# Performance work log

Measured on AMD Instinct MI355X. Metric: run time of the kernel, lower is better.

Reference implementation:

```python
import jax, jax.numpy as jnp
import numpy as np

N_DRUG = 25000
N_DIS = 25000
N = N_DRUG + N_DIS
E = 800000
D_IN = 128
D_OUT = 128


def setup_inputs() -> dict:
    key = jax.random.key(0)
    k1, k2, k3, k4, k5, k6 = jax.random.split(key, 6)
    drug_f = jax.random.normal(k1, (N_DRUG, D_IN), dtype=jnp.float32)
    disease_f = jax.random.normal(k2, (N_DIS, D_IN), dtype=jnp.float32)
    rows = jax.random.randint(k3, (E,), 0, N, dtype=jnp.int64)
    cols = jax.random.randint(k4, (E,), 0, N, dtype=jnp.int64)
    # xavier_uniform_ equivalent for [D_IN, D_OUT]
    limit = float(np.sqrt(6.0 / (D_IN + D_OUT)))
    drug_w = jax.random.uniform(k5, (D_IN, D_OUT), minval=-limit, maxval=limit, dtype=jnp.float32)
    disease_w = jax.random.uniform(k6, (D_IN, D_OUT), minval=-limit, maxval=limit, dtype=jnp.float32)
    return {"drug_f": drug_f, "disease_f": disease_f, "drug_w": drug_w,
            "disease_w": disease_w, "rows": rows, "cols": cols}


def reference(drug_f, disease_f, drug_w, disease_w, rows, cols):
    # per-type linear projection
    drug_h = drug_f @ drug_w          # [n_drug, D_OUT]
    dis_h = disease_f @ disease_w     # [n_dis,  D_OUT]
    node_f = jnp.concatenate([drug_h, dis_h], axis=0)  # [N, D_OUT]
    # row-sum degrees of the (unit-valued) sparse adjacency, clamped at 1
    deg = jax.ops.segment_sum(jnp.ones((rows.shape[0],), node_f.dtype), rows,
                              num_segments=N)
    norm = jnp.clip(deg, 1.0, None) ** -0.5           # [N]
    # symmetric norm: norm * (A @ (norm * x)); SpMM as gather + segment_sum
    node_f = node_f * norm[:, None]
    msgs = node_f[cols]                               # [E, D_OUT]
    node_f = jax.ops.segment_sum(msgs, rows, num_segments=N)
    node_f = node_f * norm[:, None]
    return node_f
```

## Files before the change

kernel.cpp:

```cpp
#include <hip/hip_runtime.h>
#include <hip/hip_bf16.h>

#define D 128
#define CAP 64
#define BINSH 7
#define NSHARD 8
#define NCHUNK 384
#define PART_EDGES 4096

typedef short short8 __attribute__((ext_vector_type(8)));
typedef unsigned short ushort8 __attribute__((ext_vector_type(8)));
typedef float f32x4  __attribute__((ext_vector_type(4)));

__device__ __forceinline__ short f2bf(float x) {
    __hip_bfloat16 b = __float2bfloat16(x);
    return *reinterpret_cast<short*>(&b);
}
__device__ __forceinline__ float bf2f(unsigned short u) {
    return __uint_as_float((unsigned)u << 16);
}

__device__ __forceinline__ void wprep_block(int b16, int tid,
                                            const float* __restrict__ w0,
                                            const float* __restrict__ w1,
                                            __hip_bfloat16* __restrict__ wb) {
    int gid = b16 * 256 + tid;
    int type = gid >> 11;
    int tri  = gid & 2047;
    int lane = tri & 63;
    int ts   = tri >> 6;
    int s = ts & 3, t = ts >> 2;
    const float* W = type ? w1 : w0;
    int n = t * 16 + (lane & 15);
    int kbase = s * 32 + (lane >> 4) * 8;
    short8 v;
    #pragma unroll
    for (int j = 0; j < 8; ++j)
        v[j] = f2bf(W[(size_t)(kbase + j) * D + n]);
    *(short8*)&wb[(size_t)type * 16384 + (size_t)tri * 8] = v;
}

__global__ __launch_bounds__(256) void prep_sort_kernel(const float* __restrict__ w0,
                                                        const float* __restrict__ w1,
                                                        __hip_bfloat16* __restrict__ wb,
                                                        int* __restrict__ bincur, int nbin) {
    int b = blockIdx.x;
    if (b < 16) { wprep_block(b, threadIdx.x, w0, w1, wb); return; }
    for (int i = threadIdx.x; i < nbin; i += 256) bincur[i] = 0;
}

__global__ __launch_bounds__(256) void part_proj_kernel(
    const int* __restrict__ rows, const int* __restrict__ cols,
    int* __restrict__ bincur, unsigned int* __restrict__ payload,
    int E, int nbin, int capbin, int nparts,
    const float* __restrict__ f0, const float* __restrict__ f1,
    const __hip_bfloat16* __restrict__ wb,
    __hip_bfloat16* __restrict__ h,
    int n0, int n1, int nb0) {

    __shared__ short8 Wl[2048];
    int b = blockIdx.x;
    int t = threadIdx.x;

    if (b < nparts) {
        int* hist = (int*)&Wl[0];
        int* base = hist + 512;
        int* cur  = hist + 1024;
        int lo = b * PART_EDGES;
        int hi = lo + PART_EDGES; if (hi > E) hi = E;

        for (int i = t; i < nbin; i += 256) hist[i] = 0;
        __syncthreads();
        for (int i = lo + t; i < hi; i += 256)
            atomicAdd(&hist[rows[i] >> BINSH], 1);
        __syncthreads();
        for (int i = t; i < nbin; i += 256) {
            int c = hist[i];
            base[i] = (c > 0) ? atomicAdd(&bincur[i], c) : 0;
            cur[i] = 0;
        }
        __syncthreads();
        for (int i = lo + t; i < hi; i += 256) {
            int r = rows[i];
            int bn = r >> BINSH;
            int p = base[bn] + atomicAdd(&cur[bn], 1);
            if (p < capbin)
                payload[(size_t)bn * capbin + p] = ((unsigned)r << 16) | (unsigned)(cols[i] & 0xffff);
        }
        return;
    }

    int pb = b - nparts;
    int type = (pb >= nb0) ? 1 : 0;
    const float* f = type ? f1 : f0;
    int lbase = (type ? (pb - nb0) : pb) * 64;
    int nloc  = type ? n1 : n0;
    int goff  = type ? n0 : 0;

    const short8* src = (const short8*)wb + (size_t)type * 2048;
    for (int i = t; i < 2048; i += 256) Wl[i] = src[i];
    __syncthreads();

    int wave = t >> 6;
    int lane = t & 63;
    int m  = lane & 15;
    int kg = lane >> 4;
    int wrow = lbase + wave * 16;

    int arow = wrow + m;
    int arc = (arow < nloc) ? arow : (nloc - 1);
    const float* fr = f + (size_t)arc * D + kg * 8;
    short8 A[4];
    #pragma unroll
    for (int s = 0; s < 4; ++s) {
        float4 x = *(const float4*)(fr + s * 32);
        float4 y = *(const float4*)(fr + s * 32 + 4);
        short8 a;
        a[0] = f2bf(x.x); a[1] = f2bf(x.y); a[2] = f2bf(x.z); a[3] = f2bf(x.w);
        a[4] = f2bf(y.x); a[5] = f2bf(y.y); a[6] = f2bf(y.z); a[7] = f2bf(y.w);
        A[s] = a;
    }

    #pragma unroll
    for (int tt = 0; tt < 8; ++tt) {
        f32x4 acc = {0.f, 0.f, 0.f, 0.f};
        #pragma unroll
        for (int s = 0; s < 4; ++s)
            acc = __builtin_amdgcn_mfma_f32_16x16x32_bf16(A[s], Wl[(tt * 4 + s) * 64 + lane], acc, 0, 0, 0);
        #pragma unroll
        for (int r = 0; r < 4; ++r) {
            int grow = wrow + kg * 4 + r;
            if (grow < nloc)
                h[(size_t)(goff + grow) * D + tt * 16 + m] = __float2bfloat16(acc[r]);
        }
    }
}

__global__ __launch_bounds__(256) void binfill_kernel(const unsigned int* __restrict__ payload,
                                                      const int* __restrict__ bincur,
                                                      unsigned short* __restrict__ bucket,
                                                      int* __restrict__ cnt,
                                                      float* __restrict__ normf,
                                                      int capbin, int N) {
    __shared__ int rc[128];
    int b = blockIdx.x;
    int t = threadIdx.x;
    if (t < 128) rc[t] = 0;
    __syncthreads();
    int cntb = bincur[b]; if (cntb > capbin) cntb = capbin;
    const unsigned int* pp = payload + (size_t)b * capbin;
    for (int i = t; i < cntb; i += 256) {
        unsigned pay = pp[i];
        int rl = (pay >> 16) & 127;
        int p = atomicAdd(&rc[rl], 1);
        if (p < CAP)
            bucket[(size_t)((b << BINSH) | rl) * CAP + p] = (unsigned short)(pay & 0xffff);
    }
    __syncthreads();
    if (t < 128) {
        int r = (b << BINSH) | t;
        if (r < N) {
            int c = rc[t];
            cnt[r] = c;
            normf[r] = rsqrtf((float)(c < 1 ? 1 : c));
        }
    }
}

__global__ __launch_bounds__(256) void agg_kernel(const int* __restrict__ cnt,
                                                  const float* __restrict__ normf,
                                                  const unsigned short* __restrict__ bucket,
                                                  const __hip_bfloat16* __restrict__ h,
                                                  float* __restrict__ out, int n) {
    int wave = threadIdx.x >> 6;
    int lane = threadIdx.x & 63;
    int r = blockIdx.x * 4 + wave;
    if (r >= n) return;
    int d = cnt[r]; if (d > CAP) d = CAP;
    int s = r * CAP;

    int col = (int)bucket[s + lane];
    int cs  = (lane < d) ? col : 0;
    float wl = (lane < d) ? normf[cs] : 0.f;

    int g  = lane >> 4;
    int sl = lane & 15;

    float acc[8] = {0.f,0.f,0.f,0.f,0.f,0.f,0.f,0.f};
    for (int j = 0; j < d; j += 4) {
        int e = j + g;
        float we = __shfl(wl, e & 63); if (e >= d) we = 0.f;
        int   ce = __shfl(cs, e & 63);
        ushort8 v = *(const ushort8*)&h[(size_t)ce * D + sl * 8];
        #pragma unroll
        for (int k = 0; k < 8; ++k)
            acc[k] += we * bf2f(v[k]);
    }
    #pragma unroll
    for (int k = 0; k < 8; ++k) {
        acc[k] += __shfl_xor(acc[k], 16);
        acc[k] += __shfl_xor(acc[k], 32);
    }
    if (g == 0) {
        float nr = normf[r];
        float* po = &out[(size_t)r * D + sl * 8];
        *(float4*)po       = make_float4(acc[0]*nr, acc[1]*nr, acc[2]*nr, acc[3]*nr);
        *(float4*)(po + 4) = make_float4(acc[4]*nr, acc[5]*nr, acc[6]*nr, acc[7]*nr);
    }
}

__global__ __launch_bounds__(256) void prep_kernel(const float* __restrict__ w0,
                                                   const float* __restrict__ w1,
                                                   __hip_bfloat16* __restrict__ wb,
                                                   int* __restrict__ cnt, int N) {
    int b = blockIdx.x;
    if (b < 16) { wprep_block(b, threadIdx.x, w0, w1, wb); }
    else {
        int i = (b - 16) * 256 + threadIdx.x;
        if (i < N) cnt[i] = 0;
    }
}

__global__ __launch_bounds__(256) void fill_shard_kernel(const int* __restrict__ rows,
                                                         const int* __restrict__ cols,
                                                         int* __restrict__ cnt,
                                                         unsigned short* __restrict__ bucket,
                                                         int E, int shsz, int ch) {
    int s     = blockIdx.x & (NSHARD - 1);
    int chunk = blockIdx.x >> 3;
    int lo = chunk * ch;
    int hi = lo + ch; if (hi > E) hi = E;
    int rlo = s * shsz;
    for (int i = lo + (int)threadIdx.x; i < hi; i += 256) {
        int r = rows[i];
        if ((unsigned)(r - rlo) < (unsigned)shsz) {
            int p = atomicAdd(&cnt[r], 1);
            if (p < CAP) bucket[(size_t)r * CAP + p] = (unsigned short)cols[i];
        }
    }
}

__global__ void norm_from_cnt_kernel(const int* __restrict__ cnt, float* __restrict__ normf, int N) {
    int i = blockIdx.x * 256 + threadIdx.x;
    if (i < N) { int c = cnt[i]; normf[i] = rsqrtf((float)(c < 1 ? 1 : c)); }
}

extern "C" void kernel_launch(void* const* d_in, const int* in_sizes, int n_in,
                              void* d_out, int out_size, void* d_ws, size_t ws_size,
                              hipStream_t stream) {
    const float* drug_f    = (const float*)d_in[0];
    const float* disease_f = (const float*)d_in[1];
    const float* drug_w    = (const float*)d_in[2];
    const float* disease_w = (const float*)d_in[3];
    const int*   rows      = (const int*)d_in[4];
    const int*   cols      = (const int*)d_in[5];
    float* out = (float*)d_out;

    int n_drug = in_sizes[0] / D;
    int n_dis  = in_sizes[1] / D;
    int N = n_drug + n_dis;
    int E = in_sizes[4];
    (void)out_size; (void)n_in;

    char* ws = (char*)d_ws;
    size_t off = 0;
    auto alloc = [&](size_t bytes) { void* p = ws + off; off = (off + bytes + 255) & ~(size_t)255; return p; };

    int*            cnt      = (int*)alloc(sizeof(int) * N);
    float*          normf    = (float*)alloc(sizeof(float) * N);
    __hip_bfloat16* h_raw    = (__hip_bfloat16*)alloc(sizeof(__hip_bfloat16) * (size_t)N * D);
    __hip_bfloat16* wb       = (__hip_bfloat16*)alloc(sizeof(__hip_bfloat16) * 2 * 16384);
    unsigned short* bucket   = (unsigned short*)alloc((size_t)N * CAP * sizeof(unsigned short));

    int nb0 = (n_drug + 63) / 64;
    int nb1 = (n_dis + 63) / 64;

    int nbin   = (N + (1 << BINSH) - 1) >> BINSH;
    int capbin = (((E / nbin) * 3 / 2) + 63) & ~63;
    size_t sort_need = off
        + ((sizeof(int) * nbin + 255) & ~(size_t)255)
        + ((sizeof(unsigned int) * (size_t)nbin * capbin + 255) & ~(size_t)255);

    if (ws_size >= sort_need && nbin <= 512) {
        int*          bincur  = (int*)alloc(sizeof(int) * nbin);
        unsigned int* payload = (unsigned int*)alloc(sizeof(unsigned int) * (size_t)nbin * capbin);

        int nparts = (E + PART_EDGES - 1) / PART_EDGES;
        prep_sort_kernel<<<17, 256, 0, stream>>>(drug_w, disease_w, wb, bincur, nbin);
        part_proj_kernel<<<nparts + nb0 + nb1, 256, 0, stream>>>(
            rows, cols, bincur, payload, E, nbin, capbin, nparts,
            drug_f, disease_f, wb, h_raw, n_drug, n_dis, nb0);
        binfill_kernel<<<nbin, 256, 0, stream>>>(payload, bincur, bucket, cnt, normf, capbin, N);
        agg_kernel<<<(N + 3) / 4, 256, 0, stream>>>(cnt, normf, bucket, h_raw, out, N);
    } else {
        int shsz = (N + NSHARD - 1) / NSHARD;
        int ch   = (E + NCHUNK - 1) / NCHUNK;
        int prep_blocks = 16 + (N + 255) / 256;

        prep_kernel<<<prep_blocks, 256, 0, stream>>>(drug_w, disease_w, wb, cnt, N);
        fill_shard_kernel<<<NCHUNK * NSHARD, 256, 0, stream>>>(rows, cols, cnt, bucket, E, shsz, ch);
        norm_from_cnt_kernel<<<(N + 255) / 256, 256, 0, stream>>>(cnt, normf, N);
        part_proj_kernel<<<nb0 + nb1, 256, 0, stream>>>(
            rows, cols, (int*)nullptr, (unsigned int*)nullptr, E, nbin, capbin, 0,
            drug_f, disease_f, wb, h_raw, n_drug, n_dis, nb0);
        agg_kernel<<<(N + 3) / 4, 256, 0, stream>>>(cnt, normf, bucket, h_raw, out, N);
    }
}
```

Before: 71.17 us.

## Use nontemporal loads/stores for streamed data and stage bucket fill in LDS

Streamed single-use data (rows, cols, features, payload, bucket, output) now goes through nontemporal load and store builtins, so it is less likely to evict the reused projected features h from cache. binfill now scatters each bin's columns into a zeroed shared-memory tile and writes the whole 128x64 bucket block out with coalesced vector stores, instead of scattered 2-byte global writes. This adds 16KB of LDS per block, which may lower occupancy, and writes the full tile including unused slots.

```diff
diff --git a/kernel.cpp b/kernel.cpp
--- a/kernel.cpp
+++ b/kernel.cpp
@@ -72,7 +72,7 @@
         for (int i = t; i < nbin; i += 256) hist[i] = 0;
         __syncthreads();
         for (int i = lo + t; i < hi; i += 256)
-            atomicAdd(&hist[rows[i] >> BINSH], 1);
+            atomicAdd(&hist[__builtin_nontemporal_load(&rows[i]) >> BINSH], 1);
         __syncthreads();
         for (int i = t; i < nbin; i += 256) {
             int c = hist[i];
@@ -81,11 +81,12 @@
         }
         __syncthreads();
         for (int i = lo + t; i < hi; i += 256) {
-            int r = rows[i];
+            int r = __builtin_nontemporal_load(&rows[i]);
+            int c = __builtin_nontemporal_load(&cols[i]);
             int bn = r >> BINSH;
             int p = base[bn] + atomicAdd(&cur[bn], 1);
             if (p < capbin)
-                payload[(size_t)bn * capbin + p] = ((unsigned)r << 16) | (unsigned)(cols[i] & 0xffff);
+                payload[(size_t)bn * capbin + p] = ((unsigned)r << 16) | (unsigned)(c & 0xffff);
         }
         return;
     }
@@ -113,11 +114,11 @@
     short8 A[4];
     #pragma unroll
     for (int s = 0; s < 4; ++s) {
-        float4 x = *(const float4*)(fr + s * 32);
-        float4 y = *(const float4*)(fr + s * 32 + 4);
+        f32x4 x = __builtin_nontemporal_load((const f32x4*)(fr + s * 32));
+        f32x4 y = __builtin_nontemporal_load((const f32x4*)(fr + s * 32 + 4));
         short8 a;
-        a[0] = f2bf(x.x); a[1] = f2bf(x.y); a[2] = f2bf(x.z); a[3] = f2bf(x.w);
-        a[4] = f2bf(y.x); a[5] = f2bf(y.y); a[6] = f2bf(y.z); a[7] = f2bf(y.w);
+        a[0] = f2bf(x[0]); a[1] = f2bf(x[1]); a[2] = f2bf(x[2]); a[3] = f2bf(x[3]);
+        a[4] = f2bf(y[0]); a[5] = f2bf(y[1]); a[6] = f2bf(y[2]); a[7] = f2bf(y[3]);
         A[s] = a;
     }
 
@@ -142,21 +143,26 @@
                                                       int* __restrict__ cnt,
                                                       float* __restrict__ normf,
                                                       int capbin, int N) {
+    __shared__ unsigned short lb[128 * CAP];
     __shared__ int rc[128];
     int b = blockIdx.x;
     int t = threadIdx.x;
     if (t < 128) rc[t] = 0;
+    ushort8 z = {0, 0, 0, 0, 0, 0, 0, 0};
+    for (int i = t; i < 1024; i += 256) ((ushort8*)lb)[i] = z;
     __syncthreads();
     int cntb = bincur[b]; if (cntb > capbin) cntb = capbin;
     const unsigned int* pp = payload + (size_t)b * capbin;
     for (int i = t; i < cntb; i += 256) {
-        unsigned pay = pp[i];
+        unsigned pay = __builtin_nontemporal_load(&pp[i]);
         int rl = (pay >> 16) & 127;
         int p = atomicAdd(&rc[rl], 1);
         if (p < CAP)
-            bucket[(size_t)((b << BINSH) | rl) * CAP + p] = (unsigned short)(pay & 0xffff);
+            lb[rl * CAP + p] = (unsigned short)(pay & 0xffff);
     }
     __syncthreads();
+    ushort8* gb = (ushort8*)(bucket + (((size_t)b << BINSH) * CAP));
+    for (int i = t; i < 1024; i += 256) gb[i] = ((ushort8*)lb)[i];
     if (t < 128) {
         int r = (b << BINSH) | t;
         if (r < N) {
@@ -179,7 +185,7 @@
     int d = cnt[r]; if (d > CAP) d = CAP;
     int s = r * CAP;
 
-    int col = (int)bucket[s + lane];
+    int col = (int)__builtin_nontemporal_load(&bucket[s + lane]);
     int cs  = (lane < d) ? col : 0;
     float wl = (lane < d) ? normf[cs] : 0.f;
 
@@ -204,8 +210,10 @@
     if (g == 0) {
         float nr = normf[r];
         float* po = &out[(size_t)r * D + sl * 8];
-        *(float4*)po       = make_float4(acc[0]*nr, acc[1]*nr, acc[2]*nr, acc[3]*nr);
-        *(float4*)(po + 4) = make_float4(acc[4]*nr, acc[5]*nr, acc[6]*nr, acc[7]*nr);
+        f32x4 o0 = {acc[0]*nr, acc[1]*nr, acc[2]*nr, acc[3]*nr};
+        f32x4 o1 = {acc[4]*nr, acc[5]*nr, acc[6]*nr, acc[7]*nr};
+        __builtin_nontemporal_store(o0, (f32x4*)po);
+        __builtin_nontemporal_store(o1, (f32x4*)(po + 4));
     }
 }
 
```

New measurement: 78.61 us. 10.4% more time.
